# Kernel tuning notes

Measured on AMD Instinct MI355X. Metric: run time of the kernel, lower is better.

The kernel has to match this reference:

```python
import jax, jax.numpy as jnp
import numpy as np

N_POINTS = 692736  # B * N_cams * D * fH * fW = 4*6*41*16*44
C_FEAT = 64


def setup_inputs() -> dict:
    key = jax.random.key(0)
    k_x, k_gx, k_gy, k_gb = jax.random.split(key, 4)
    B, nx, ny, nz = 4, 256, 256, 1
    x = jax.random.normal(k_x, (N_POINTS, C_FEAT), dtype=jnp.float32)
    # voxel coords (ix, iy, iz, batch) all in-range (LSS filters out-of-range points upstream)
    gx = jax.random.randint(k_gx, (N_POINTS,), 0, nx)
    gy = jax.random.randint(k_gy, (N_POINTS,), 0, ny)
    gz = jnp.zeros((N_POINTS,), dtype=jnp.int32)
    gb = jax.random.randint(k_gb, (N_POINTS,), 0, B)
    geom_feats = jnp.stack([gx.astype(jnp.int32), gy.astype(jnp.int32), gz, gb.astype(jnp.int32)], axis=1)
    return {"x": x, "geom_feats": geom_feats, "B": B, "nx": nx, "ny": ny, "nz": nz}


def reference(x, geom_feats, B, nx, ny, nz):
    # Linearized voxel rank, exactly as LiftSplatShoot.voxel_pooling:
    # ranks = gx*(B*ny*nz) + gy*(B*nz) + gz*B + gb
    g = geom_feats.astype(jnp.int32)
    ranks = g[:, 0] * (B * ny * nz) + g[:, 1] * (B * nz) + g[:, 2] * B + g[:, 3]
    # voxel_pooling sorts points by rank before cumsum_trick
    order = jnp.argsort(ranks)
    x_s = x[order]
    ranks_s = ranks[order]
    # cumsum_trick = cumsum + segment-boundary mask + diff  ==  per-voxel sum.
    # segment_sum computes the identical reduction with a fixed output shape.
    num_voxels = B * nx * ny * nz
    pooled = jax.ops.segment_sum(x_s, ranks_s, num_segments=num_voxels)  # [nx*ny*nz*B, C]
    # Scatter into dense BEV grid: final[b, c, z, ix, iy] = pooled
    final = pooled.reshape(nx, ny, nz, B, -1)          # [nx, ny, nz, B, C]
    final = jnp.transpose(final, (3, 4, 2, 0, 1))       # [B, C, nz, nx, ny]
    Bn, C, Z, X, Y = final.shape
    # collapse Z into channels (torch.cat(final.unbind(dim=2), 1))
    return final.reshape(Bn, C * Z, X, Y)
```

## Files before the change

### kernel.cpp

```cpp
#include <hip/hip_runtime.h>
#include <hip/hip_bf16.h>


#define NPTS   692736
#define CFEAT  64
#define NXV    256
#define NYV    256
#define NBAT   4
#define NVOX   (NBAT * NXV * NYV)


__device__ __forceinline__ int voxel_of(const int* __restrict__ geom, int i) {
    const int4 g = *(const int4*)(geom + (size_t)i * 4);
    return (g.w * NXV + g.x) * NYV + g.y;
}

__global__ __launch_bounds__(256) void count_kernel(
    const int* __restrict__ geom, int* __restrict__ count)
{
    int i = blockIdx.x * 256 + threadIdx.x;
    atomicAdd(&count[voxel_of(geom, i)], 1);
}

__global__ __launch_bounds__(256) void scan_block_kernel(
    const int* __restrict__ count, int* __restrict__ offsets,
    int* __restrict__ blockSums)
{
    int tid = threadIdx.x;
    int base = blockIdx.x * 1024 + tid * 4;
    int4 c = *(const int4*)(count + base);
    int s = c.x + c.y + c.z + c.w;

    int lane = tid & 63, wave = tid >> 6;
    int incl = s;
    #pragma unroll
    for (int d = 1; d < 64; d <<= 1) {
        int t = __shfl_up(incl, d, 64);
        if (lane >= d) incl += t;
    }
    __shared__ int waveSum[4];
    if (lane == 63) waveSum[wave] = incl;
    __syncthreads();
    int waveBase = 0;
    #pragma unroll
    for (int w = 0; w < 3; ++w) if (w < wave) waveBase += waveSum[w];

    int excl = waveBase + incl - s;
    int4 o;
    o.x = excl; o.y = excl + c.x; o.z = o.y + c.y; o.w = o.z + c.z;
    *(int4*)(offsets + base) = o;
    if (tid == 255) blockSums[blockIdx.x] = waveBase + incl;
}

__global__ __launch_bounds__(256) void scan_top_kernel(
    const int* __restrict__ blockSums, int* __restrict__ blockBase)
{
    int tid = threadIdx.x;
    int s = blockSums[tid];
    int lane = tid & 63, wave = tid >> 6;
    int incl = s;
    #pragma unroll
    for (int d = 1; d < 64; d <<= 1) {
        int t = __shfl_up(incl, d, 64);
        if (lane >= d) incl += t;
    }
    __shared__ int waveSum[4];
    if (lane == 63) waveSum[wave] = incl;
    __syncthreads();
    int waveBase = 0;
    #pragma unroll
    for (int w = 0; w < 3; ++w) if (w < wave) waveBase += waveSum[w];
    blockBase[tid] = waveBase + incl - s;
}

__global__ __launch_bounds__(256) void finalize_kernel(
    int* __restrict__ offsets, const int* __restrict__ blockBase,
    int* __restrict__ cursor)
{
    int v = blockIdx.x * 256 + threadIdx.x;
    int off = offsets[v] + blockBase[v >> 10];
    offsets[v] = off;
    cursor[v]  = off;
}

__global__ __launch_bounds__(256) void fill_idx_kernel(
    const int* __restrict__ geom, int* __restrict__ cursor,
    int* __restrict__ idx)
{
    int i = blockIdx.x * 256 + threadIdx.x;
    int v = voxel_of(geom, i);
    int pos = atomicAdd(&cursor[v], 1);
    idx[pos] = i;
}

__global__ __launch_bounds__(512) void gather_kernel(
    const float* __restrict__ x, const int* __restrict__ offsets,
    const int* __restrict__ cursor, const int* __restrict__ idx,
    float* __restrict__ out)
{
    int b  = blockIdx.x >> 8;
    int ix = blockIdx.x & 255;
    int iy = threadIdx.x & 255;
    int h  = threadIdx.x >> 8;

    int v = (b * NXV + ix) * NYV + iy;
    int k   = offsets[v];
    int end = cursor[v];

    float4 acc[8] = {};
    for (; k < end; ++k) {
        int p = idx[k];
        const float4* row = (const float4*)(x + (size_t)p * CFEAT + h * 32);
        #pragma unroll
        for (int q = 0; q < 8; ++q) {
            float4 f = row[q];
            acc[q].x += f.x; acc[q].y += f.y; acc[q].z += f.z; acc[q].w += f.w;
        }
    }

    size_t obase = (((size_t)b * CFEAT + h * 32) * NXV + ix) * NYV + iy;
    #pragma unroll
    for (int q = 0; q < 8; ++q) {
        out[obase + (size_t)(q * 4 + 0) * (NXV * NYV)] = acc[q].x;
        out[obase + (size_t)(q * 4 + 1) * (NXV * NYV)] = acc[q].y;
        out[obase + (size_t)(q * 4 + 2) * (NXV * NYV)] = acc[q].z;
        out[obase + (size_t)(q * 4 + 3) * (NXV * NYV)] = acc[q].w;
    }
}

extern "C" void kernel_launch(void* const* d_in, const int* in_sizes, int n_in,
                              void* d_out, int out_size, void* d_ws, size_t ws_size,
                              hipStream_t stream) {
    const float* x  = (const float*)d_in[0];
    const int* geom = (const int*)d_in[1];
    float* out      = (float*)d_out;

    char* w = (char*)d_ws;
    int* count     = (int*)(w);
    int* offsets   = (int*)(w + (1u << 20));
    int* cursor    = (int*)(w + (2u << 20));
    int* blockSums = (int*)(w + (3u << 20));
    int* blockBase = (int*)(w + (3u << 20) + 4096);
    int* idx       = (int*)(w + (4u << 20));

    hipMemsetAsync(count, 0, NVOX * sizeof(int), stream);

    count_kernel   <<<NPTS / 256, 256, 0, stream>>>(geom, count);
    scan_block_kernel<<<NVOX / 1024, 256, 0, stream>>>(count, offsets, blockSums);
    scan_top_kernel<<<1, 256, 0, stream>>>(blockSums, blockBase);
    finalize_kernel<<<NVOX / 256, 256, 0, stream>>>(offsets, blockBase, cursor);
    fill_idx_kernel<<<NPTS / 256, 256, 0, stream>>>(geom, cursor, idx);
    gather_kernel  <<<NBAT * NXV, 512, 0, stream>>>(x, offsets, cursor, idx, out);
}
```

Before: 375.0 us.

## Replace counting-sort scan pipeline with fixed-capacity voxel buckets plus overflow list

Drops the count/scan/finalize passes and the second atomic pass by writing each point's index directly into a fixed 16-slot bucket per voxel. Points beyond capacity go to a global overflow list that the gather kernel scans linearly for affected voxels. Gather loads now use nontemporal hints for x and the output stores. This cuts kernel launches and one full pass over geometry, but risks slow linear overflow scans if voxel occupancy is skewed. It also uses a larger bucket workspace.

```diff
diff --git a/kernel.cpp b/kernel.cpp
--- a/kernel.cpp
+++ b/kernel.cpp
@@ -1,5 +1,4 @@
 #include <hip/hip_runtime.h>
-#include <hip/hip_bf16.h>
 
 
 #define NPTS   692736
@@ -8,6 +7,9 @@
 #define NYV    256
 #define NBAT   4
 #define NVOX   (NBAT * NXV * NYV)
+#define CAP    16
+
+typedef float f32x4 __attribute__((ext_vector_type(4)));
 
 
 __device__ __forceinline__ int voxel_of(const int* __restrict__ geom, int i) {
@@ -15,116 +17,66 @@
     return (g.w * NXV + g.x) * NYV + g.y;
 }
 
-__global__ __launch_bounds__(256) void count_kernel(
-    const int* __restrict__ geom, int* __restrict__ count)
-{
-    int i = blockIdx.x * 256 + threadIdx.x;
-    atomicAdd(&count[voxel_of(geom, i)], 1);
-}
-
-__global__ __launch_bounds__(256) void scan_block_kernel(
-    const int* __restrict__ count, int* __restrict__ offsets,
-    int* __restrict__ blockSums)
-{
-    int tid = threadIdx.x;
-    int base = blockIdx.x * 1024 + tid * 4;
-    int4 c = *(const int4*)(count + base);
-    int s = c.x + c.y + c.z + c.w;
-
-    int lane = tid & 63, wave = tid >> 6;
-    int incl = s;
-    #pragma unroll
-    for (int d = 1; d < 64; d <<= 1) {
-        int t = __shfl_up(incl, d, 64);
-        if (lane >= d) incl += t;
-    }
-    __shared__ int waveSum[4];
-    if (lane == 63) waveSum[wave] = incl;
-    __syncthreads();
-    int waveBase = 0;
-    #pragma unroll
-    for (int w = 0; w < 3; ++w) if (w < wave) waveBase += waveSum[w];
-
-    int excl = waveBase + incl - s;
-    int4 o;
-    o.x = excl; o.y = excl + c.x; o.z = o.y + c.y; o.w = o.z + c.z;
-    *(int4*)(offsets + base) = o;
-    if (tid == 255) blockSums[blockIdx.x] = waveBase + incl;
-}
-
-__global__ __launch_bounds__(256) void scan_top_kernel(
-    const int* __restrict__ blockSums, int* __restrict__ blockBase)
-{
-    int tid = threadIdx.x;
-    int s = blockSums[tid];
-    int lane = tid & 63, wave = tid >> 6;
-    int incl = s;
-    #pragma unroll
-    for (int d = 1; d < 64; d <<= 1) {
-        int t = __shfl_up(incl, d, 64);
-        if (lane >= d) incl += t;
-    }
-    __shared__ int waveSum[4];
-    if (lane == 63) waveSum[wave] = incl;
-    __syncthreads();
-    int waveBase = 0;
-    #pragma unroll
-    for (int w = 0; w < 3; ++w) if (w < wave) waveBase += waveSum[w];
-    blockBase[tid] = waveBase + incl - s;
-}
-
-__global__ __launch_bounds__(256) void finalize_kernel(
-    int* __restrict__ offsets, const int* __restrict__ blockBase,
-    int* __restrict__ cursor)
-{
-    int v = blockIdx.x * 256 + threadIdx.x;
-    int off = offsets[v] + blockBase[v >> 10];
-    offsets[v] = off;
-    cursor[v]  = off;
-}
-
-__global__ __launch_bounds__(256) void fill_idx_kernel(
-    const int* __restrict__ geom, int* __restrict__ cursor,
-    int* __restrict__ idx)
+__global__ __launch_bounds__(256) void fill_kernel(
+    const int* __restrict__ geom, int* __restrict__ count,
+    int* __restrict__ bucket, int* __restrict__ ovf_cnt, int* __restrict__ ovf)
 {
     int i = blockIdx.x * 256 + threadIdx.x;
     int v = voxel_of(geom, i);
-    int pos = atomicAdd(&cursor[v], 1);
-    idx[pos] = i;
+    int pos = atomicAdd(&count[v], 1);
+    if (pos < CAP) {
+        bucket[(size_t)v * CAP + pos] = i;
+    } else {
+        int j = atomicAdd(ovf_cnt, 1);
+        ovf[2 * j]     = v;
+        ovf[2 * j + 1] = i;
+    }
 }
 
 __global__ __launch_bounds__(512) void gather_kernel(
-    const float* __restrict__ x, const int* __restrict__ offsets,
-    const int* __restrict__ cursor, const int* __restrict__ idx,
-    float* __restrict__ out)
+    const float* __restrict__ x, const int* __restrict__ count,
+    const int* __restrict__ bucket, const int* __restrict__ ovf_cnt,
+    const int* __restrict__ ovf, float* __restrict__ out)
 {
     int b  = blockIdx.x >> 8;
     int ix = blockIdx.x & 255;
     int iy = threadIdx.x & 255;
     int h  = threadIdx.x >> 8;
 
-    int v = (b * NXV + ix) * NYV + iy;
-    int k   = offsets[v];
-    int end = cursor[v];
+    int v   = (b * NXV + ix) * NYV + iy;
+    int cnt = count[v];
+    int n   = cnt < CAP ? cnt : CAP;
+    const int* __restrict__ bk = bucket + (size_t)v * CAP;
 
-    float4 acc[8] = {};
-    for (; k < end; ++k) {
-        int p = idx[k];
-        const float4* row = (const float4*)(x + (size_t)p * CFEAT + h * 32);
+    f32x4 acc[8] = {};
+    for (int k = 0; k < n; ++k) {
+        int p = bk[k];
+        const f32x4* row = (const f32x4*)(x + (size_t)p * CFEAT + h * 32);
         #pragma unroll
-        for (int q = 0; q < 8; ++q) {
-            float4 f = row[q];
-            acc[q].x += f.x; acc[q].y += f.y; acc[q].z += f.z; acc[q].w += f.w;
+        for (int q = 0; q < 8; ++q)
+            acc[q] += __builtin_nontemporal_load(row + q);
+    }
+
+    if (cnt > CAP) {
+        int no = *ovf_cnt;
+        for (int j = 0; j < no; ++j) {
+            if (ovf[2 * j] == v) {
+                int p = ovf[2 * j + 1];
+                const f32x4* row = (const f32x4*)(x + (size_t)p * CFEAT + h * 32);
+                #pragma unroll
+                for (int q = 0; q < 8; ++q)
+                    acc[q] += row[q];
+            }
         }
     }
 
     size_t obase = (((size_t)b * CFEAT + h * 32) * NXV + ix) * NYV + iy;
     #pragma unroll
     for (int q = 0; q < 8; ++q) {
-        out[obase + (size_t)(q * 4 + 0) * (NXV * NYV)] = acc[q].x;
-        out[obase + (size_t)(q * 4 + 1) * (NXV * NYV)] = acc[q].y;
-        out[obase + (size_t)(q * 4 + 2) * (NXV * NYV)] = acc[q].z;
-        out[obase + (size_t)(q * 4 + 3) * (NXV * NYV)] = acc[q].w;
+        #pragma unroll
+        for (int j = 0; j < 4; ++j)
+            __builtin_nontemporal_store(acc[q][j],
+                out + obase + (size_t)(q * 4 + j) * (NXV * NYV));
     }
 }
 
@@ -136,19 +88,13 @@
     float* out      = (float*)d_out;
 
     char* w = (char*)d_ws;
-    int* count     = (int*)(w);
-    int* offsets   = (int*)(w + (1u << 20));
-    int* cursor    = (int*)(w + (2u << 20));
-    int* blockSums = (int*)(w + (3u << 20));
-    int* blockBase = (int*)(w + (3u << 20) + 4096);
-    int* idx       = (int*)(w + (4u << 20));
+    int* count   = (int*)(w);
+    int* ovf_cnt = (int*)(w + (1u << 20));
+    int* ovf     = (int*)(w + (1u << 20) + 64);
+    int* bucket  = (int*)(w + (8u << 20));
 
-    hipMemsetAsync(count, 0, NVOX * sizeof(int), stream);
+    hipMemsetAsync(w, 0, (1u << 20) + 64, stream);
 
-    count_kernel   <<<NPTS / 256, 256, 0, stream>>>(geom, count);
-    scan_block_kernel<<<NVOX / 1024, 256, 0, stream>>>(count, offsets, blockSums);
-    scan_top_kernel<<<1, 256, 0, stream>>>(blockSums, blockBase);
-    finalize_kernel<<<NVOX / 256, 256, 0, stream>>>(offsets, blockBase, cursor);
-    fill_idx_kernel<<<NPTS / 256, 256, 0, stream>>>(geom, cursor, idx);
-    gather_kernel  <<<NBAT * NXV, 512, 0, stream>>>(x, offsets, cursor, idx, out);
+    fill_kernel  <<<NPTS / 256, 256, 0, stream>>>(geom, count, bucket, ovf_cnt, ovf);
+    gather_kernel<<<NBAT * NXV, 512, 0, stream>>>(x, count, bucket, ovf_cnt, ovf, out);
 }
```

Result: slower. 397.6 us (+6.0%).
